# Optimization experiments

Measured on AMD Instinct MI355X. Metric: run time of the kernel, lower is better.

## Reference

```python
import jax, jax.numpy as jnp
import numpy as np

N = 50000
D = 128
E = 800000
L = 3


def setup_inputs() -> dict:
    key = jax.random.key(0)
    ks = jax.random.split(key, 6)
    z = jax.random.normal(ks[0], (N, D), dtype=jnp.float32)
    edge_index = jax.random.randint(ks[1], (2, E), 0, N, dtype=jnp.int64)
    s1 = 1.0 / np.sqrt(2 * D)
    s2 = 1.0 / np.sqrt(D)
    # per-layer MLP params, stacked over layers: y = x @ W + b (W stored input-major)
    W1 = jax.random.uniform(ks[2], (L, 2 * D, D), jnp.float32, -s1, s1)
    b1 = jax.random.uniform(ks[3], (L, D), jnp.float32, -s1, s1)
    W2 = jax.random.uniform(ks[4], (L, D, D), jnp.float32, -s2, s2)
    b2 = jax.random.uniform(ks[5], (L, D), jnp.float32, -s2, s2)
    return {"z": z, "edge_index": edge_index, "W1": W1, "b1": b1, "W2": W2, "b2": b2}


def _edgeconv(h, src, dst, W1, b1, W2, b2):
    # message: mlp(cat[x_i, x_j]) per edge; x_i = target (dst), x_j = source (src)
    tmp = jnp.concatenate([h[dst], h[src]], axis=1)           # [E, 2D]
    m = jax.nn.relu(tmp @ W1 + b1) @ W2 + b2                  # [E, D]
    agg = jax.ops.segment_max(m, dst, num_segments=N)          # [N, D], -inf for empty
    return jnp.where(jnp.isfinite(agg), agg, 0.0)


def reference(z, edge_index, W1, b1, W2, b2):
    src = edge_index[0]
    dst = edge_index[1]
    h = z
    for l in range(L - 1):
        h = jax.nn.relu(_edgeconv(h, src, dst, W1[l], b1[l], W2[l], b2[l]))
    h = _edgeconv(h, src, dst, W1[L - 1], b1[L - 1], W2[L - 1], b2[L - 1])
    return h
```

## Files before the change

kernel.cpp:

```cpp
#include <hip/hip_runtime.h>

#define DH 128
#define NLAYER 3
typedef unsigned short ushort_t;
typedef __attribute__((ext_vector_type(8))) short bf16x8;
typedef __attribute__((ext_vector_type(4))) float f32x4;

__device__ __forceinline__ ushort_t f2bf(float a) {
    unsigned u = __float_as_uint(a);
    return (ushort_t)((u + 0x7fffu + ((u >> 16) & 1u)) >> 16);
}
__device__ __forceinline__ float bf2f(ushort_t h) {
    return __uint_as_float(((unsigned)h) << 16);
}

__device__ __forceinline__ unsigned enc_f(float f) {
    unsigned u = __float_as_uint(f);
    return (u & 0x80000000u) ? ~u : (u | 0x80000000u);
}
__device__ __forceinline__ float dec_f(unsigned u) {
    unsigned b = (u & 0x80000000u) ? (u ^ 0x80000000u) : ~u;
    return __uint_as_float(b);
}
#define ENC_NEG_INF 0x007FFFFFu

__global__ void fill_u(unsigned* __restrict__ p, int n, unsigned v) {
    int i = blockIdx.x * blockDim.x + threadIdx.x;
    int stride = gridDim.x * blockDim.x;
    for (; i < n; i += stride) p[i] = v;
}

__global__ void hist_kernel(const int* __restrict__ dst, unsigned* __restrict__ cnt, int E) {
    int e = blockIdx.x * blockDim.x + threadIdx.x;
    int stride = gridDim.x * blockDim.x;
    for (; e < E; e += stride) atomicAdd(&cnt[dst[e]], 1u);
}

__global__ __launch_bounds__(1024) void scan_local(const unsigned* __restrict__ cnt,
                                                   unsigned* __restrict__ off,
                                                   unsigned* __restrict__ bsum, int n) {
    __shared__ unsigned s[1024];
    const int t = threadIdx.x;
    int idx = blockIdx.x * 1024 + t;
    unsigned v = (idx < n) ? cnt[idx] : 0u;
    s[t] = v;
    __syncthreads();
    for (int d = 1; d < 1024; d <<= 1) {
        unsigned u = (t >= d) ? s[t - d] : 0u;
        __syncthreads();
        s[t] += u;
        __syncthreads();
    }
    if (idx < n) off[idx] = s[t] - v;
    if (t == 1023) bsum[blockIdx.x] = s[t];
}
__global__ void scan_base(unsigned* __restrict__ bsum, int nb) {
    __shared__ unsigned s[64];
    const int t = threadIdx.x;
    unsigned v = (t < nb) ? bsum[t] : 0u;
    s[t] = v;
    __syncthreads();
    for (int d = 1; d < 64; d <<= 1) {
        unsigned u = (t >= d) ? s[t - d] : 0u;
        __syncthreads();
        s[t] += u;
        __syncthreads();
    }
    if (t < nb) bsum[t] = s[t] - v;
}
__global__ void scan_add(unsigned* __restrict__ off, const unsigned* __restrict__ bsum,
                         unsigned* __restrict__ cnt, int n) {
    int i = blockIdx.x * blockDim.x + threadIdx.x;
    int stride = gridDim.x * blockDim.x;
    for (; i < n; i += stride) { off[i] += bsum[i >> 10]; cnt[i] = 0u; }
}

__global__ void scatter_kernel(const int* __restrict__ src, const int* __restrict__ dst,
                               const unsigned* __restrict__ off, unsigned* __restrict__ cur,
                               int* __restrict__ s_src, int* __restrict__ s_dst, int E) {
    int e = blockIdx.x * blockDim.x + threadIdx.x;
    int stride = gridDim.x * blockDim.x;
    for (; e < E; e += stride) {
        int d = dst[e];
        unsigned p = off[d] + atomicAdd(&cur[d], 1u);
        s_src[p] = src[e];
        s_dst[p] = d;
    }
}

__global__ void convert_w(const float* __restrict__ W1, const float* __restrict__ W2,
                          ushort_t* __restrict__ W1t_hi, ushort_t* __restrict__ W1t_lo,
                          ushort_t* __restrict__ W2t_hi, ushort_t* __restrict__ W2t_lo) {
    const int T1 = NLAYER * 256 * DH, T2 = NLAYER * DH * DH;
    int i = blockIdx.x * blockDim.x + threadIdx.x;
    int stride = gridDim.x * blockDim.x;
    for (; i < T1 + T2; i += stride) {
        if (i < T1) {
            int l = i >> 15, r = i & 32767, c = r >> 7, k = r & 127;
            float w = W1[(size_t)l * 32768 + (size_t)((c < 128) ? k : 128 + k) * DH + (c & 127)];
            ushort_t hi = f2bf(w);
            W1t_hi[i] = hi; W1t_lo[i] = f2bf(w - bf2f(hi));
        } else {
            int j = i - T1;
            int l = j >> 14, r = j & 16383, c = r >> 7, k = r & 127;
            float w = W2[(size_t)l * 16384 + (size_t)k * DH + c];
            ushort_t hi = f2bf(w);
            W2t_hi[j] = hi; W2t_lo[j] = f2bf(w - bf2f(hi));
        }
    }
}

__global__ void convert_h(const float* __restrict__ z, unsigned* __restrict__ hpk, int n) {
    int i = blockIdx.x * blockDim.x + threadIdx.x;
    int stride = gridDim.x * blockDim.x;
    for (; i < n; i += stride) {
        float a = z[i];
        ushort_t hi = f2bf(a);
        ushort_t lo = f2bf(a - bf2f(hi));
        hpk[i] = (unsigned)hi | ((unsigned)lo << 16);
    }
}

__global__ __launch_bounds__(256, 2) void node_gemm(
    const unsigned* __restrict__ hpk,
    const ushort_t* __restrict__ wthi, const ushort_t* __restrict__ wtlo,
    const float* __restrict__ bias, float* __restrict__ outp, int N) {
    __shared__ char smem[65536];
    char* Whi = smem;
    char* Wlo = smem + 32768;
    const int t = threadIdx.x;
    const int w = t >> 6, l = t & 63;
    for (int cid = t; cid < 2048; cid += 256) {
        int c = cid >> 4, ch = cid & 15;
        uint4 vh = *(const uint4*)(wthi + (size_t)cid * 8);
        uint4 vl = *(const uint4*)(wtlo + (size_t)cid * 8);
        *(uint4*)(Whi + c * 256 + ((ch ^ (c & 15)) << 4)) = vh;
        *(uint4*)(Wlo + c * 256 + ((ch ^ (c & 15)) << 4)) = vl;
    }
    const int n0 = blockIdx.x * 128;
    bf16x8 ahi[2][4], alo[2][4];
    #pragma unroll
    for (int rt = 0; rt < 2; ++rt) {
        int row = n0 + w * 32 + rt * 16 + (l & 15);
        if (row >= N) row = N - 1;
        const unsigned* ph = hpk + (size_t)row * DH + 8 * (l >> 4);
        #pragma unroll
        for (int ks = 0; ks < 4; ++ks) {
            uint4 p0 = *(const uint4*)(ph + ks * 32);
            uint4 p1 = *(const uint4*)(ph + ks * 32 + 4);
            bf16x8 hv, lv;
            hv[0] = (short)(p0.x & 0xffffu); lv[0] = (short)(p0.x >> 16);
            hv[1] = (short)(p0.y & 0xffffu); lv[1] = (short)(p0.y >> 16);
            hv[2] = (short)(p0.z & 0xffffu); lv[2] = (short)(p0.z >> 16);
            hv[3] = (short)(p0.w & 0xffffu); lv[3] = (short)(p0.w >> 16);
            hv[4] = (short)(p1.x & 0xffffu); lv[4] = (short)(p1.x >> 16);
            hv[5] = (short)(p1.y & 0xffffu); lv[5] = (short)(p1.y >> 16);
            hv[6] = (short)(p1.z & 0xffffu); lv[6] = (short)(p1.z >> 16);
            hv[7] = (short)(p1.w & 0xffffu); lv[7] = (short)(p1.w >> 16);
            ahi[rt][ks] = hv; alo[rt][ks] = lv;
        }
    }
    f32x4 acc[2][8];
    #pragma unroll
    for (int rt = 0; rt < 2; ++rt)
        #pragma unroll
        for (int ct = 0; ct < 8; ++ct) acc[rt][ct] = (f32x4){0.f, 0.f, 0.f, 0.f};
    __syncthreads();
    #pragma unroll
    for (int ct = 0; ct < 8; ++ct) {
        int colv = ct * 16 + (l & 15);
        #pragma unroll
        for (int ks = 0; ks < 4; ++ks) {
            int chb = ks * 4 + (l >> 4);
            int addr = colv * 256 + ((chb ^ (colv & 15)) << 4);
            bf16x8 bh = *(const bf16x8*)(Whi + addr);
            bf16x8 bl = *(const bf16x8*)(Wlo + addr);
            #pragma unroll
            for (int rt = 0; rt < 2; ++rt) {
                acc[rt][ct] = __builtin_amdgcn_mfma_f32_16x16x32_bf16(ahi[rt][ks], bh, acc[rt][ct], 0, 0, 0);
                acc[rt][ct] = __builtin_amdgcn_mfma_f32_16x16x32_bf16(ahi[rt][ks], bl, acc[rt][ct], 0, 0, 0);
                acc[rt][ct] = __builtin_amdgcn_mfma_f32_16x16x32_bf16(alo[rt][ks], bh, acc[rt][ct], 0, 0, 0);
            }
        }
    }
    #pragma unroll
    for (int ct = 0; ct < 8; ++ct) {
        int col = ct * 16 + (l & 15);
        float bv = bias ? bias[col] : 0.0f;
        #pragma unroll
        for (int rt = 0; rt < 2; ++rt)
            #pragma unroll
            for (int i = 0; i < 4; ++i) {
                int row = n0 + w * 32 + rt * 16 + (l >> 4) * 4 + i;
                if (row < N) outp[(size_t)row * DH + col] = acc[rt][ct][i] + bv;
            }
    }
}

__global__ __launch_bounds__(256, 2) void edge_mlp(
    const float* __restrict__ Afp, const float* __restrict__ Bfp,
    const int* __restrict__ src, const int* __restrict__ dst,
    const ushort_t* __restrict__ w2hi, const ushort_t* __restrict__ w2lo,
    unsigned* __restrict__ agg, int E) {
    __shared__ char smem[66048];
    char* Whi = smem;
    char* Wlo = smem + 32768;
    int* sdst = (int*)(smem + 65536);
    float* R = (float*)smem;
    const int t = threadIdx.x;
    const int w = t >> 6, l = t & 63;
    const int e0 = blockIdx.x * 128;

    bf16x8 ahi[2][4], alo[2][4];
    #pragma unroll
    for (int rt = 0; rt < 2; ++rt) {
        int er = w * 32 + rt * 16 + (l & 15);
        int dn = dst[e0 + er], sn = src[e0 + er];
        const float* pa = Afp + (size_t)dn * DH + 8 * (l >> 4);
        const float* pb = Bfp + (size_t)sn * DH + 8 * (l >> 4);
        #pragma unroll
        for (int ks = 0; ks < 4; ++ks) {
            float4 a0 = *(const float4*)(pa + ks * 32);
            float4 a1 = *(const float4*)(pa + ks * 32 + 4);
            float4 b0 = *(const float4*)(pb + ks * 32);
            float4 b1 = *(const float4*)(pb + ks * 32 + 4);
            float v0 = fmaxf(a0.x + b0.x, 0.f), v1 = fmaxf(a0.y + b0.y, 0.f);
            float v2 = fmaxf(a0.z + b0.z, 0.f), v3 = fmaxf(a0.w + b0.w, 0.f);
            float v4 = fmaxf(a1.x + b1.x, 0.f), v5 = fmaxf(a1.y + b1.y, 0.f);
            float v6 = fmaxf(a1.z + b1.z, 0.f), v7 = fmaxf(a1.w + b1.w, 0.f);
            ushort_t h0 = f2bf(v0), h1 = f2bf(v1), h2 = f2bf(v2), h3 = f2bf(v3);
            ushort_t h4 = f2bf(v4), h5 = f2bf(v5), h6 = f2bf(v6), h7 = f2bf(v7);
            bf16x8 hv, lv;
            hv[0] = (short)h0; lv[0] = (short)f2bf(v0 - bf2f(h0));
            hv[1] = (short)h1; lv[1] = (short)f2bf(v1 - bf2f(h1));
            hv[2] = (short)h2; lv[2] = (short)f2bf(v2 - bf2f(h2));
            hv[3] = (short)h3; lv[3] = (short)f2bf(v3 - bf2f(h3));
            hv[4] = (short)h4; lv[4] = (short)f2bf(v4 - bf2f(h4));
            hv[5] = (short)h5; lv[5] = (short)f2bf(v5 - bf2f(h5));
            hv[6] = (short)h6; lv[6] = (short)f2bf(v6 - bf2f(h6));
            hv[7] = (short)h7; lv[7] = (short)f2bf(v7 - bf2f(h7));
            ahi[rt][ks] = hv; alo[rt][ks] = lv;
        }
    }
    if (t < 128) sdst[t] = dst[e0 + t];
    for (int cid = t; cid < 2048; cid += 256) {
        int c = cid >> 4, ch = cid & 15;
        uint4 vh = *(const uint4*)(w2hi + (size_t)cid * 8);
        uint4 vl = *(const uint4*)(w2lo + (size_t)cid * 8);
        *(uint4*)(Whi + c * 256 + ((ch ^ (c & 15)) << 4)) = vh;
        *(uint4*)(Wlo + c * 256 + ((ch ^ (c & 15)) << 4)) = vl;
    }
    f32x4 acc[2][8];
    #pragma unroll
    for (int rt = 0; rt < 2; ++rt)
        #pragma unroll
        for (int ct = 0; ct < 8; ++ct) acc[rt][ct] = (f32x4){0.f, 0.f, 0.f, 0.f};
    __syncthreads();
    #pragma unroll
    for (int ct = 0; ct < 8; ++ct) {
        int colv = ct * 16 + (l & 15);
        #pragma unroll
        for (int ks = 0; ks < 4; ++ks) {
            int chb = ks * 4 + (l >> 4);
            int addr = colv * 256 + ((chb ^ (colv & 15)) << 4);
            bf16x8 bh = *(const bf16x8*)(Whi + addr);
            bf16x8 bl = *(const bf16x8*)(Wlo + addr);
            #pragma unroll
            for (int rt = 0; rt < 2; ++rt) {
                acc[rt][ct] = __builtin_amdgcn_mfma_f32_16x16x32_bf16(ahi[rt][ks], bh, acc[rt][ct], 0, 0, 0);
                acc[rt][ct] = __builtin_amdgcn_mfma_f32_16x16x32_bf16(ahi[rt][ks], bl, acc[rt][ct], 0, 0, 0);
                acc[rt][ct] = __builtin_amdgcn_mfma_f32_16x16x32_bf16(alo[rt][ks], bh, acc[rt][ct], 0, 0, 0);
            }
        }
    }
    #pragma unroll
    for (int chh = 0; chh < 2; ++chh) {
        __syncthreads();
        #pragma unroll
        for (int rt = 0; rt < 2; ++rt)
            #pragma unroll
            for (int c4 = 0; c4 < 4; ++c4) {
                int ct = chh * 4 + c4;
                int col64 = c4 * 16 + (l & 15);
                #pragma unroll
                for (int i = 0; i < 4; ++i) {
                    int row = w * 32 + rt * 16 + (l >> 4) * 4 + i;
                    R[row * 64 + (col64 ^ (((row >> 2) & 3) << 4))] = acc[rt][ct][i];
                }
            }
        __syncthreads();
        const int col = l;
        const int r0 = w * 32;
        float run = R[r0 * 64 + (col ^ (((r0 >> 2) & 3) << 4))];
        int cur = sdst[r0];
        #pragma unroll
        for (int rr = r0 + 1; rr < r0 + 32; ++rr) {
            float x = R[rr * 64 + (col ^ (((rr >> 2) & 3) << 4))];
            int dd = sdst[rr];
            if (dd != cur) {
                atomicMax(&agg[(size_t)cur * DH + chh * 64 + col], enc_f(run));
                cur = dd; run = x;
            } else {
                run = fmaxf(run, x);
            }
        }
        atomicMax(&agg[(size_t)cur * DH + chh * 64 + col], enc_f(run));
    }
}

__global__ void finalize_kernel(unsigned* agg, const float* __restrict__ b2,
                                unsigned* hpk, float* __restrict__ outf, int n, int mode) {
    int i = blockIdx.x * blockDim.x + threadIdx.x;
    int stride = gridDim.x * blockDim.x;
    for (; i < n; i += stride) {
        unsigned uv = agg[i];
        float f = (uv == ENC_NEG_INF) ? 0.0f : dec_f(uv) + b2[i & (DH - 1)];
        if (mode == 0) {
            f = fmaxf(f, 0.0f);
            ushort_t hi = f2bf(f);
            ushort_t lo = f2bf(f - bf2f(hi));
            hpk[i] = (unsigned)hi | ((unsigned)lo << 16);
        } else {
            outf[i] = f;
        }
    }
}

extern "C" void kernel_launch(void* const* d_in, const int* in_sizes, int n_in,
                              void* d_out, int out_size, void* d_ws, size_t ws_size,
                              hipStream_t stream) {
    const float* z  = (const float*)d_in[0];
    const int*   ei = (const int*)d_in[1];
    const float* W1 = (const float*)d_in[2];
    const float* b1 = (const float*)d_in[3];
    const float* W2 = (const float*)d_in[4];
    const float* b2 = (const float*)d_in[5];
    const int N = 50000, D = DH, E = 800000;
    const int* srcp = ei;
    const int* dstp = ei + E;

    float* Abuf = (float*)d_ws;
    float* Bbuf = Abuf + (size_t)N * D;
    unsigned* agg = (unsigned*)(Bbuf + (size_t)N * D);
    ushort_t* W1t_hi = (ushort_t*)(agg + (size_t)N * D);
    ushort_t* W1t_lo = W1t_hi + NLAYER * 256 * D;
    ushort_t* W2t_hi = W1t_lo + NLAYER * 256 * D;
    ushort_t* W2t_lo = W2t_hi + NLAYER * D * D;
    unsigned* cnt = (unsigned*)(W2t_lo + NLAYER * D * D);
    unsigned* off = cnt + N;
    unsigned* bsum = off + N;
    int* s_src = (int*)(bsum + 64);
    int* s_dst = s_src + E;
    float* outp = (float*)d_out;

    convert_w<<<128, 256, 0, stream>>>(W1, W2, W1t_hi, W1t_lo, W2t_hi, W2t_lo);
    convert_h<<<1024, 256, 0, stream>>>(z, agg, N * D);

    const int NB = (N + 1023) / 1024;
    fill_u<<<256, 256, 0, stream>>>(cnt, N, 0u);
    hist_kernel<<<1024, 256, 0, stream>>>(dstp, cnt, E);
    scan_local<<<NB, 1024, 0, stream>>>(cnt, off, bsum, N);
    scan_base<<<1, 64, 0, stream>>>(bsum, NB);
    scan_add<<<256, 256, 0, stream>>>(off, bsum, cnt, N);
    scatter_kernel<<<1024, 256, 0, stream>>>(srcp, dstp, off, cnt, s_src, s_dst, E);

    const int nrb = (N + 127) / 128;
    for (int l = 0; l < NLAYER; ++l) {
        node_gemm<<<nrb, 256, 0, stream>>>(agg, W1t_hi + ((size_t)l * 256) * D,
                                           W1t_lo + ((size_t)l * 256) * D,
                                           b1 + (size_t)l * D, Abuf, N);
        node_gemm<<<nrb, 256, 0, stream>>>(agg, W1t_hi + ((size_t)l * 256 + 128) * D,
                                           W1t_lo + ((size_t)l * 256 + 128) * D,
                                           nullptr, Bbuf, N);
        fill_u<<<2048, 256, 0, stream>>>(agg, N * D, ENC_NEG_INF);
        edge_mlp<<<E / 128, 256, 0, stream>>>(Abuf, Bbuf, s_src, s_dst,
                                              W2t_hi + (size_t)l * D * D,
                                              W2t_lo + (size_t)l * D * D, agg, E);
        finalize_kernel<<<2048, 256, 0, stream>>>(agg, b2 + (size_t)l * D,
                                                  agg, outp, N * D,
                                                  (l < NLAYER - 1) ? 0 : 1);
    }
}
```

Before: 893.9 us.

## Halve edge MLP shared memory via two-phase W2 load, merge node GEMMs

Edge MLP now stages W2 into shared memory in two 64-column halves, cutting LDS per block roughly in half so more blocks can be resident per CU. The W2 load is also issued before the edge gathers, so it can overlap them. Hi/lo bf16 splitting now uses the packed v_cvt_pk_bf16_f32 instruction. The two node GEMM launches are merged into one grid that picks its weight half by block index. In exchange, the kernel pays an extra barrier and a second weight load per block.

```diff
diff --git a/kernel.cpp b/kernel.cpp
--- a/kernel.cpp
+++ b/kernel.cpp
@@ -12,6 +12,11 @@
 }
 __device__ __forceinline__ float bf2f(ushort_t h) {
     return __uint_as_float(((unsigned)h) << 16);
+}
+__device__ __forceinline__ unsigned cvtpk(float a, float b) {
+    unsigned r;
+    asm("v_cvt_pk_bf16_f32 %0, %1, %2" : "=v"(r) : "v"(a), "v"(b));
+    return r;
 }
 
 __device__ __forceinline__ unsigned enc_f(float f) {
@@ -124,20 +129,26 @@
 __global__ __launch_bounds__(256, 2) void node_gemm(
     const unsigned* __restrict__ hpk,
     const ushort_t* __restrict__ wthi, const ushort_t* __restrict__ wtlo,
-    const float* __restrict__ bias, float* __restrict__ outp, int N) {
+    const float* __restrict__ bias, float* __restrict__ outA, float* __restrict__ outB,
+    int N, int nrb) {
     __shared__ char smem[65536];
     char* Whi = smem;
     char* Wlo = smem + 32768;
+    const int bb = blockIdx.x;
+    const int half = (bb >= nrb) ? 1 : 0;
+    const ushort_t* whi = wthi + (half ? (size_t)128 * DH : 0);
+    const ushort_t* wlo = wtlo + (half ? (size_t)128 * DH : 0);
+    float* outp = half ? outB : outA;
     const int t = threadIdx.x;
     const int w = t >> 6, l = t & 63;
     for (int cid = t; cid < 2048; cid += 256) {
         int c = cid >> 4, ch = cid & 15;
-        uint4 vh = *(const uint4*)(wthi + (size_t)cid * 8);
-        uint4 vl = *(const uint4*)(wtlo + (size_t)cid * 8);
+        uint4 vh = *(const uint4*)(whi + (size_t)cid * 8);
+        uint4 vl = *(const uint4*)(wlo + (size_t)cid * 8);
         *(uint4*)(Whi + c * 256 + ((ch ^ (c & 15)) << 4)) = vh;
         *(uint4*)(Wlo + c * 256 + ((ch ^ (c & 15)) << 4)) = vl;
     }
-    const int n0 = blockIdx.x * 128;
+    const int n0 = (bb - half * nrb) * 128;
     bf16x8 ahi[2][4], alo[2][4];
     #pragma unroll
     for (int rt = 0; rt < 2; ++rt) {
@@ -186,7 +197,7 @@
     #pragma unroll
     for (int ct = 0; ct < 8; ++ct) {
         int col = ct * 16 + (l & 15);
-        float bv = bias ? bias[col] : 0.0f;
+        float bv = half ? 0.0f : bias[col];
         #pragma unroll
         for (int rt = 0; rt < 2; ++rt)
             #pragma unroll
@@ -202,14 +213,24 @@
     const int* __restrict__ src, const int* __restrict__ dst,
     const ushort_t* __restrict__ w2hi, const ushort_t* __restrict__ w2lo,
     unsigned* __restrict__ agg, int E) {
-    __shared__ char smem[66048];
-    char* Whi = smem;
-    char* Wlo = smem + 32768;
-    int* sdst = (int*)(smem + 65536);
+    __shared__ char smem[33280];
+    int* sdst = (int*)(smem + 32768);
     float* R = (float*)smem;
     const int t = threadIdx.x;
     const int w = t >> 6, l = t & 63;
     const int e0 = blockIdx.x * 128;
+
+    if (t < 128) sdst[t] = dst[e0 + t];
+    #pragma unroll
+    for (int i = 0; i < 4; ++i) {
+        int cid = i * 256 + t;
+        int cc = cid >> 4, ch = cid & 15;
+        int sc = ch ^ (cc & 15);
+        uint4 vh = *(const uint4*)(w2hi + (size_t)cc * DH + sc * 8);
+        uint4 vl = *(const uint4*)(w2lo + (size_t)cc * DH + sc * 8);
+        *(uint4*)(smem + cid * 16) = vh;
+        *(uint4*)(smem + 16384 + cid * 16) = vl;
+    }
 
     bf16x8 ahi[2][4], alo[2][4];
     #pragma unroll
@@ -228,27 +249,23 @@
             float v2 = fmaxf(a0.z + b0.z, 0.f), v3 = fmaxf(a0.w + b0.w, 0.f);
             float v4 = fmaxf(a1.x + b1.x, 0.f), v5 = fmaxf(a1.y + b1.y, 0.f);
             float v6 = fmaxf(a1.z + b1.z, 0.f), v7 = fmaxf(a1.w + b1.w, 0.f);
-            ushort_t h0 = f2bf(v0), h1 = f2bf(v1), h2 = f2bf(v2), h3 = f2bf(v3);
-            ushort_t h4 = f2bf(v4), h5 = f2bf(v5), h6 = f2bf(v6), h7 = f2bf(v7);
-            bf16x8 hv, lv;
-            hv[0] = (short)h0; lv[0] = (short)f2bf(v0 - bf2f(h0));
-            hv[1] = (short)h1; lv[1] = (short)f2bf(v1 - bf2f(h1));
-            hv[2] = (short)h2; lv[2] = (short)f2bf(v2 - bf2f(h2));
-            hv[3] = (short)h3; lv[3] = (short)f2bf(v3 - bf2f(h3));
-            hv[4] = (short)h4; lv[4] = (short)f2bf(v4 - bf2f(h4));
-            hv[5] = (short)h5; lv[5] = (short)f2bf(v5 - bf2f(h5));
-            hv[6] = (short)h6; lv[6] = (short)f2bf(v6 - bf2f(h6));
-            hv[7] = (short)h7; lv[7] = (short)f2bf(v7 - bf2f(h7));
-            ahi[rt][ks] = hv; alo[rt][ks] = lv;
-        }
-    }
-    if (t < 128) sdst[t] = dst[e0 + t];
-    for (int cid = t; cid < 2048; cid += 256) {
-        int c = cid >> 4, ch = cid & 15;
-        uint4 vh = *(const uint4*)(w2hi + (size_t)cid * 8);
-        uint4 vl = *(const uint4*)(w2lo + (size_t)cid * 8);
-        *(uint4*)(Whi + c * 256 + ((ch ^ (c & 15)) << 4)) = vh;
-        *(uint4*)(Wlo + c * 256 + ((ch ^ (c & 15)) << 4)) = vl;
+            unsigned h01 = cvtpk(v0, v1), h23 = cvtpk(v2, v3);
+            unsigned h45 = cvtpk(v4, v5), h67 = cvtpk(v6, v7);
+            float l0 = v0 - __uint_as_float(h01 << 16);
+            float l1 = v1 - __uint_as_float(h01 & 0xffff0000u);
+            float l2 = v2 - __uint_as_float(h23 << 16);
+            float l3 = v3 - __uint_as_float(h23 & 0xffff0000u);
+            float l4 = v4 - __uint_as_float(h45 << 16);
+            float l5 = v5 - __uint_as_float(h45 & 0xffff0000u);
+            float l6 = v6 - __uint_as_float(h67 << 16);
+            float l7 = v7 - __uint_as_float(h67 & 0xffff0000u);
+            unsigned q01 = cvtpk(l0, l1), q23 = cvtpk(l2, l3);
+            unsigned q45 = cvtpk(l4, l5), q67 = cvtpk(l6, l7);
+            uint4 hp = {h01, h23, h45, h67};
+            uint4 lp = {q01, q23, q45, q67};
+            ahi[rt][ks] = *(bf16x8*)&hp;
+            alo[rt][ks] = *(bf16x8*)&lp;
+        }
     }
     f32x4 acc[2][8];
     #pragma unroll
@@ -257,14 +274,43 @@
         for (int ct = 0; ct < 8; ++ct) acc[rt][ct] = (f32x4){0.f, 0.f, 0.f, 0.f};
     __syncthreads();
     #pragma unroll
-    for (int ct = 0; ct < 8; ++ct) {
+    for (int ct = 0; ct < 4; ++ct) {
         int colv = ct * 16 + (l & 15);
         #pragma unroll
         for (int ks = 0; ks < 4; ++ks) {
             int chb = ks * 4 + (l >> 4);
             int addr = colv * 256 + ((chb ^ (colv & 15)) << 4);
-            bf16x8 bh = *(const bf16x8*)(Whi + addr);
-            bf16x8 bl = *(const bf16x8*)(Wlo + addr);
+            bf16x8 bh = *(const bf16x8*)(smem + addr);
+            bf16x8 bl = *(const bf16x8*)(smem + 16384 + addr);
+            #pragma unroll
+            for (int rt = 0; rt < 2; ++rt) {
+                acc[rt][ct] = __builtin_amdgcn_mfma_f32_16x16x32_bf16(ahi[rt][ks], bh, acc[rt][ct], 0, 0, 0);
+                acc[rt][ct] = __builtin_amdgcn_mfma_f32_16x16x32_bf16(ahi[rt][ks], bl, acc[rt][ct], 0, 0, 0);
+                acc[rt][ct] = __builtin_amdgcn_mfma_f32_16x16x32_bf16(alo[rt][ks], bh, acc[rt][ct], 0, 0, 0);
+            }
+        }
+    }
+    __syncthreads();
+    #pragma unroll
+    for (int i = 0; i < 4; ++i) {
+        int cid = i * 256 + t;
+        int cc = cid >> 4, ch = cid & 15;
+        int sc = ch ^ (cc & 15);
+        uint4 vh = *(const uint4*)(w2hi + (size_t)(64 + cc) * DH + sc * 8);
+        uint4 vl = *(const uint4*)(w2lo + (size_t)(64 + cc) * DH + sc * 8);
+        *(uint4*)(smem + cid * 16) = vh;
+        *(uint4*)(smem + 16384 + cid * 16) = vl;
+    }
+    __syncthreads();
+    #pragma unroll
+    for (int ct = 4; ct < 8; ++ct) {
+        int colv = ct * 16 + (l & 15);
+        #pragma unroll
+        for (int ks = 0; ks < 4; ++ks) {
+            int chb = ks * 4 + (l >> 4);
+            int addr = (colv & 63) * 256 + ((chb ^ (colv & 15)) << 4);
+            bf16x8 bh = *(const bf16x8*)(smem + addr);
+            bf16x8 bl = *(const bf16x8*)(smem + 16384 + addr);
             #pragma unroll
             for (int rt = 0; rt < 2; ++rt) {
                 acc[rt][ct] = __builtin_amdgcn_mfma_f32_16x16x32_bf16(ahi[rt][ks], bh, acc[rt][ct], 0, 0, 0);
@@ -366,12 +412,10 @@
 
     const int nrb = (N + 127) / 128;
     for (int l = 0; l < NLAYER; ++l) {
-        node_gemm<<<nrb, 256, 0, stream>>>(agg, W1t_hi + ((size_t)l * 256) * D,
-                                           W1t_lo + ((size_t)l * 256) * D,
-                                           b1 + (size_t)l * D, Abuf, N);
-        node_gemm<<<nrb, 256, 0, stream>>>(agg, W1t_hi + ((size_t)l * 256 + 128) * D,
-                                           W1t_lo + ((size_t)l * 256 + 128) * D,
-                                           nullptr, Bbuf, N);
+        node_gemm<<<2 * nrb, 256, 0, stream>>>(agg,
+                                               W1t_hi + ((size_t)l * 256) * D,
+                                               W1t_lo + ((size_t)l * 256) * D,
+                                               b1 + (size_t)l * D, Abuf, Bbuf, N, nrb);
         fill_u<<<2048, 256, 0, stream>>>(agg, N * D, ENC_NEG_INF);
         edge_mlp<<<E / 128, 256, 0, stream>>>(Abuf, Bbuf, s_src, s_dst,
                                               W2t_hi + (size_t)l * D * D,
```

Result: faster. 782.3 us (-12.5%).
